# Kernel tuning notes

Measured on AMD Instinct MI355X. Metric: run time of the kernel, lower is better.

Reference implementation:

```python
import jax, jax.numpy as jnp
import numpy as np

SIZE = 416
STRIDES = (8, 16, 32)
A = 3            # anchors per scale
C = 20           # num classes
CONF_THRESH = 0.001
NMS_THRESH = 0.5
ANCHORS = [[1.0,1.5],[2.0,3.0],[3.0,2.5],[1.5,3.5],[3.0,4.0],[4.0,3.0],[3.5,5.0],[5.0,4.5],[8.0,8.0]]


def _make_grids():
    # Mirrors myYOLOv3.init_grid, including the off-by-one that leaves the
    # LAST cell of each scale with zero anchor_wh (slice start:index).
    anchors = np.asarray(ANCHORS, np.float32).reshape(3, 3, 2)
    anchors = anchors * np.array([4.0, 2.0, 1.0], np.float32).reshape(3, 1, 1)
    grids, awhs, strs = [], [], []
    for i, s in enumerate(STRIDES):
        ws, hs = SIZE // s, SIZE // s
        ys, xs = np.meshgrid(np.arange(hs), np.arange(ws), indexing='ij')
        g = np.stack([xs, ys], -1).reshape(hs * ws, 1, 2).astype(np.float32)
        grids.append(np.broadcast_to(g, (hs * ws, A, 2)))
        awh = np.broadcast_to(anchors[i], (hs * ws, A, 2)).copy()
        awh[hs * ws - 1] = 0.0  # replicate init_grid bug
        awhs.append(awh)
        strs.append(np.full((hs * ws, A), s, np.float32))
    grid = jnp.asarray(np.concatenate(grids, 0))      # [HWt, A, 2]
    awh = jnp.asarray(np.concatenate(awhs, 0))        # [HWt, A, 2]
    stride = jnp.asarray(np.concatenate(strs, 0).reshape(-1))  # [HWt*A]
    return grid, awh, stride


def _flatten(pred):
    # [B, A*(1+C+4), H, W] -> obj [B, HW*A], cls [B, HW*A, C], xywh [B, HW, A, 4]
    B, abC, H, W = pred.shape
    p = jnp.transpose(pred, (0, 2, 3, 1)).reshape(B, H * W, abC)
    obj = p[..., :A].reshape(B, H * W * A)
    cls = p[..., A:A * (1 + C)].reshape(B, H * W * A, C)
    xywh = p[..., A * (1 + C):].reshape(B, H * W, A, 4)
    return obj, cls, xywh


def _nms(boxes, scores, cls_inds, valid):
    # Greedy per-class NMS: processing in global score order and suppressing
    # only same-class overlaps is exactly equivalent to the per-class loops
    # in myYOLOv3.postprocess.
    N = boxes.shape[0]
    order = jnp.argsort(-scores)
    b = boxes[order]
    c = cls_inds[order]
    v = valid[order]
    areas = (b[:, 2] - b[:, 0]) * (b[:, 3] - b[:, 1])
    idx = jnp.arange(N)

    def body(i, carry):
        keep, supp = carry
        ki = v[i] & ~supp[i]
        xx1 = jnp.maximum(b[i, 0], b[:, 0])
        yy1 = jnp.maximum(b[i, 1], b[:, 1])
        xx2 = jnp.minimum(b[i, 2], b[:, 2])
        yy2 = jnp.minimum(b[i, 3], b[:, 3])
        inter = jnp.maximum(1e-28, xx2 - xx1) * jnp.maximum(1e-28, yy2 - yy1)
        iou = inter / (areas[i] + areas - inter)
        supp = supp | (ki & (iou > NMS_THRESH) & (c == c[i]) & (idx > i))
        return keep.at[i].set(ki), supp

    keep_s, _ = jax.lax.fori_loop(
        0, N, body, (jnp.zeros(N, bool), jnp.zeros(N, bool)))
    return jnp.zeros(N, bool).at[order].set(keep_s)


def setup_inputs() -> dict:
    key = jax.random.key(0)
    k1, k2, k3 = jax.random.split(key, 3)
    B, abC = 64, A * (1 + 4 + C)
    return {
        'pred_1': jax.random.normal(k1, (B, abC, 52, 52), jnp.float32),
        'pred_2': jax.random.normal(k2, (B, abC, 26, 26), jnp.float32),
        'pred_3': jax.random.normal(k3, (B, abC, 13, 13), jnp.float32),
    }


def reference(pred_1, pred_2, pred_3):
    grid, awh, stride = _make_grids()
    objs, clss, xys = zip(*[_flatten(p) for p in (pred_1, pred_2, pred_3)])
    obj = jnp.concatenate(objs, 1)    # [B, N]
    cls = jnp.concatenate(clss, 1)    # [B, N, C]
    xywh = jnp.concatenate(xys, 1)    # [B, HWt, A, 4]
    B = obj.shape[0]

    # decode_boxes: sigmoid/exp + grid add + stride scale -> xyxy pixels
    cxy = jax.nn.sigmoid(xywh[..., :2]) + grid
    bwh = jnp.exp(xywh[..., 2:]) * awh
    bbox = jnp.concatenate([cxy, bwh], -1).reshape(B, -1, 4)  # [B, N, 4]
    half = bbox[..., 2:] * 0.5
    st = stride[None, :, None]
    boxes = jnp.concatenate([(bbox[..., :2] - half) * st,
                             (bbox[..., :2] + half) * st], -1)  # [B,N,4]

    all_obj = jax.nn.sigmoid(obj[0])                 # [N]
    all_bbox = boxes[0] / SIZE                       # normalized
    all_class = jax.nn.softmax(cls[0], axis=1) * all_obj[:, None]
    cls_inds = jnp.argmax(all_class, axis=1)
    scores = jnp.max(all_class, axis=1)
    valid = scores >= CONF_THRESH

    keep = _nms(all_bbox, scores, cls_inds, valid)

    # bboxes *= scale; clip to [0, SIZE-1]; /= scale
    bboxes = jnp.clip(all_bbox * SIZE, 0.0, SIZE - 1.0) / SIZE
    return bboxes, scores, cls_inds, keep
```

## Files before the change

### kernel.cpp

```cpp
#include <hip/hip_runtime.h>
#include <stdint.h>

typedef unsigned long long u64;
typedef unsigned int u32;

#define NA 10647
#define NCLS 20
#define CAPB 1024
#define CAP2 640
#define NWP 11
#define OUT_SCORES 42588
#define OUT_CLS    53235
#define OUT_KEEP   63882

__constant__ float c_aw[9] = {4.f,8.f,12.f, 3.f,6.f,8.f, 3.5f,5.f,8.f};
__constant__ float c_ah[9] = {6.f,12.f,10.f, 7.f,8.f,6.f, 5.f,4.5f,8.f};

__device__ __forceinline__ float sig(float x){ return 1.0f/(1.0f+expf(-x)); }

__device__ __forceinline__ u64 shflxor64(u64 v, int m){
    int lo = __shfl_xor((int)(u32)(v & 0xffffffffull), m);
    int hi = __shfl_xor((int)(u32)(v >> 32), m);
    return ((u64)(u32)hi << 32) | (u32)lo;
}

__global__ void decode_kernel(const float* __restrict__ p1, const float* __restrict__ p2,
                              const float* __restrict__ p3, float* __restrict__ out,
                              float4* __restrict__ box4, u64* __restrict__ bucket,
                              int* __restrict__ cls_cnt, float* __restrict__ keep_out)
{
    int n = blockIdx.x*256 + threadIdx.x;
    if (n >= NA) return;
    const float* p; int base, W, HW, L; float s;
    if (n < 8112)      { p=p1; base=0;     W=52; HW=2704; s=8.f;  L=0; }
    else if (n<10140)  { p=p2; base=8112;  W=26; HW=676;  s=16.f; L=1; }
    else               { p=p3; base=10140; W=13; HW=169;  s=32.f; L=2; }
    int r  = n - base;
    int hw = r/3, a = r - hw*3;
    int h  = hw/W, w = hw - h*W;

    float obj = sig(p[(size_t)a*HW + hw]);

    float e[NCLS];
    #pragma unroll
    for (int c=0;c<NCLS;c++) e[c] = p[(size_t)(3 + a*NCLS + c)*HW + hw];
    float xmax = e[0];
    #pragma unroll
    for (int c=1;c<NCLS;c++) xmax = fmaxf(xmax, e[c]);
    float ssum = 0.f;
    #pragma unroll
    for (int c=0;c<NCLS;c++){ e[c] = expf(e[c]-xmax); ssum += e[c]; }
    float best = -1.0f; int bi = 0;
    #pragma unroll
    for (int c=0;c<NCLS;c++){ float v = (e[c]/ssum)*obj; if (v > best){ best=v; bi=c; } }

    int xb = 63 + a*4;
    float tx = p[(size_t)(xb+0)*HW + hw];
    float ty = p[(size_t)(xb+1)*HW + hw];
    float tw = p[(size_t)(xb+2)*HW + hw];
    float th = p[(size_t)(xb+3)*HW + hw];
    float aw = c_aw[L*3+a], ah = c_ah[L*3+a];
    if (hw == HW-1){ aw=0.f; ah=0.f; }
    float cx = sig(tx) + (float)w;
    float cy = sig(ty) + (float)h;
    float bw = expf(tw)*aw, bh = expf(th)*ah;
    float hx = bw*0.5f,  hy = bh*0.5f;
    float x1 = ((cx-hx)*s)/416.0f;
    float y1 = ((cy-hy)*s)/416.0f;
    float x2 = ((cx+hx)*s)/416.0f;
    float y2 = ((cy+hy)*s)/416.0f;

    out[n*4+0] = fminf(fmaxf(x1*416.0f,0.f),415.f)/416.0f;
    out[n*4+1] = fminf(fmaxf(y1*416.0f,0.f),415.f)/416.0f;
    out[n*4+2] = fminf(fmaxf(x2*416.0f,0.f),415.f)/416.0f;
    out[n*4+3] = fminf(fmaxf(y2*416.0f,0.f),415.f)/416.0f;
    out[OUT_SCORES + n] = best;
    out[OUT_CLS    + n] = (float)bi;

    box4[n] = make_float4(x1,y1,x2,y2);

    u64 key = ((u64)(~__float_as_uint(best)) << 32) | (u32)n;
    int pos = atomicAdd(&cls_cnt[bi], 1);
    if (pos < CAPB) bucket[(size_t)bi*CAPB + pos] = key;
    else keep_out[n] = 0.0f;
}

__global__ __launch_bounds__(512) void sort_kernel(
    const u64* __restrict__ bucket, const int* __restrict__ cls_cnt,
    const float4* __restrict__ box4, u64* __restrict__ skeys_g,
    float4* __restrict__ sbox_g)
{
    __shared__ u64 lk[CAPB];
    int b = blockIdx.x, tid = threadIdx.x;
    int cnt = cls_cnt[b];
    int Mall = (cnt < CAPB) ? cnt : CAPB;
    int M    = (cnt < CAP2) ? cnt : CAP2;
    for (int t = tid; t < CAPB; t += 512)
        lk[t] = (t < Mall) ? bucket[(size_t)b*CAPB + t] : ~0ull;
    __syncthreads();
    for (int k = 2; k <= CAPB; k <<= 1){
        for (int j = k >> 1; j > 0; j >>= 1){
            int low = tid & (j-1); int i1 = ((tid ^ low) << 1) | low; int i2 = i1 | j;
            bool asc = (i1 & k) == 0;
            u64 A = lk[i1], B = lk[i2];
            if ((A > B) == asc){ lk[i1] = B; lk[i2] = A; }
            __syncthreads();
        }
    }
    for (int t = tid; t < CAPB; t += 512) skeys_g[(size_t)b*CAPB + t] = lk[t];
    for (int t = tid; t < CAP2; t += 512){
        float4 bx = make_float4(0.f,0.f,0.f,0.f);
        if (t < M) bx = box4[(u32)lk[t]];
        sbox_g[(size_t)b*CAP2 + t] = bx;
    }
}

__global__ __launch_bounds__(256) void build_kernel(
    const float4* __restrict__ sbox_g, const int* __restrict__ cls_cnt,
    u64* __restrict__ maskg)
{
    __shared__ float4 cb_s[CAP2];
    __shared__ float  ca_s[CAP2];
    int rc = blockIdx.x, b = blockIdx.y;
    int tid = threadIdx.x, wv = tid>>6, ln = tid&63;
    int cnt = cls_cnt[b];
    int M  = (cnt < CAP2) ? cnt : CAP2;
    int MC = (M + 63) & ~63;
    if (rc*64 >= MC) return;
    for (int t = tid; t < CAP2; t += 256){
        float4 bx = sbox_g[(size_t)b*CAP2 + t];
        cb_s[t] = bx;
        ca_s[t] = (bx.z - bx.x) * (bx.w - bx.y);
    }
    __syncthreads();
    int nw = MC >> 6;
    for (int ri = wv; ri < 64; ri += 4){
        int rrow = rc*64 + ri;
        float4 rb = cb_s[rrow]; float ra = ca_s[rrow];
        for (int w = 0; w < nw; w++){
            int j = w*64 + ln;
            float4 cb = cb_s[j]; float ca = ca_s[j];
            float xx1=fmaxf(rb.x,cb.x), yy1=fmaxf(rb.y,cb.y);
            float xx2=fminf(rb.z,cb.z), yy2=fminf(rb.w,cb.w);
            float inter=fmaxf(1e-28f,xx2-xx1)*fmaxf(1e-28f,yy2-yy1);
            float iou = inter/((ra+ca)-inter);
            u64 bm = __ballot(iou > 0.5f);
            if (ln == 0) maskg[((size_t)b*CAP2 + rrow)*NWP + w] = bm;
        }
    }
}

__global__ __launch_bounds__(512) void scan_kernel(
    const u64* __restrict__ maskg, const u64* __restrict__ skeys_g,
    const int* __restrict__ cls_cnt, float* __restrict__ keep_out)
{
    __shared__ u64 lm[CAP2*NWP];
    __shared__ u64 validw_s[CAP2/64], remw[CAP2/64], keepw_s[CAP2/64];
    __shared__ u64 keep_bc;
    int b = blockIdx.x, tid = threadIdx.x, wv = tid>>6, ln = tid&63;
    int cnt = cls_cnt[b];
    int Mall = (cnt < CAPB) ? cnt : CAPB;
    int M    = (cnt < CAP2) ? cnt : CAP2;
    int MC = (M + 63) & ~63;
    int nw = MC >> 6;

    for (int t = tid; t < MC*NWP; t += 512) lm[t] = maskg[(size_t)b*CAP2*NWP + t];
    for (int w0 = wv; w0 < nw; w0 += 8){
        int t = w0*64 + ln;
        u64 key = skeys_g[(size_t)b*CAPB + t];
        float sc = __uint_as_float(~(u32)(key >> 32));
        u64 bm = __ballot(t < M && sc >= 0.001f);
        if (ln == 0) validw_s[w0] = bm;
    }
    for (int w = tid; w < nw; w += 512) remw[w] = 0ull;
    __syncthreads();

    for (int c = 0; c < nw; c++){
        if (wv == 0){
            u64 W = lm[(c*64 + ln)*NWP + c];
            u64 rem  = remw[c];
            u64 cand = validw_s[c] & ~rem;
            u64 keepw = 0;
            while (cand){
                int bp  = __builtin_ctzll(cand);
                int bps = __builtin_amdgcn_readfirstlane(bp);
                u64 rowm = ((u64)(u32)__builtin_amdgcn_readlane((int)(u32)(W>>32), bps) << 32)
                         |        (u32)__builtin_amdgcn_readlane((int)(u32)(W),     bps);
                keepw |= 1ull << bps;
                cand  &= ~(rowm | (1ull << bps));
            }
            if (ln == 0){ keepw_s[c] = keepw; keep_bc = keepw; }
        }
        __syncthreads();
        u64 kk = keep_bc;
        if (kk && c + 1 < nw){
            int i0 = tid >> 4;
            int wsl = tid & 15;
            int w = c + 1 + wsl;
            u64 acc = 0;
            if (w < nw){
                if ((kk >> i0) & 1ull)        acc  = lm[(c*64 + i0)*NWP + w];
                int i1 = i0 + 32;
                if ((kk >> i1) & 1ull)        acc |= lm[(c*64 + i1)*NWP + w];
            }
            acc |= shflxor64(acc, 16);
            acc |= shflxor64(acc, 32);
            if (ln < 16 && w < nw && acc) atomicOr(&remw[w], acc);
        }
        __syncthreads();
    }

    for (int t = tid; t < Mall; t += 512){
        u32 o = (u32)skeys_g[(size_t)b*CAPB + t];
        float kv = 0.0f;
        if (t < M) kv = ((keepw_s[t>>6] >> (t&63)) & 1ull) ? 1.0f : 0.0f;
        keep_out[o] = kv;
    }
}

extern "C" void kernel_launch(void* const* d_in, const int* in_sizes, int n_in,
                              void* d_out, int out_size, void* d_ws, size_t ws_size,
                              hipStream_t stream) {
    const float* p1 = (const float*)d_in[0];
    const float* p2 = (const float*)d_in[1];
    const float* p3 = (const float*)d_in[2];
    float* out = (float*)d_out;

    char* ws = (char*)d_ws;
    size_t off = 0;
    auto alloc = [&](size_t bytes)->void*{ void* p = ws + off; off += (bytes + 255) & ~(size_t)255; return p; };
    float4* box4    = (float4*)alloc((size_t)NA*16);
    u64*    bucket  = (u64*)   alloc((size_t)NCLS*CAPB*8);
    int*    cls_cnt = (int*)   alloc((size_t)NCLS*4);
    u64*    skeys_g = (u64*)   alloc((size_t)NCLS*CAPB*8);
    float4* sbox_g  = (float4*)alloc((size_t)NCLS*CAP2*16);
    u64*    maskg   = (u64*)   alloc((size_t)NCLS*CAP2*NWP*8);

    hipMemsetAsync(cls_cnt, 0, NCLS*sizeof(int), stream);
    decode_kernel<<<(NA+255)/256, 256, 0, stream>>>(p1,p2,p3,out,box4,bucket,cls_cnt,
                                                    out + OUT_KEEP);
    sort_kernel <<<NCLS, 512, 0, stream>>>(bucket, cls_cnt, box4, skeys_g, sbox_g);
    build_kernel<<<dim3(CAP2/64, NCLS), 256, 0, stream>>>(sbox_g, cls_cnt, maskg);
    scan_kernel <<<NCLS, 512, 0, stream>>>(maskg, skeys_g, cls_cnt, out + OUT_KEEP);
}
```

Baseline: 184.1 us.

## Sort in registers with wave shuffles for small strides, shrink decode blocks

The per-class bitonic sort now keeps one key per thread in a register across 1024 threads. It exchanges via wave64 shuffles for strides up to 32 and goes through shared memory only for larger strides. This removes most __syncthreads barriers and LDS traffic from the 55 compare-exchange steps. Decode blocks also shrink from 256 to 128 threads to spread the work over more blocks. The cost is larger sort blocks and two barriers per shared-memory stage.

After: 181.7 us. Within noise of the previous version (-1.3%).

```diff
diff --git a/kernel.cpp b/kernel.cpp
--- a/kernel.cpp
+++ b/kernel.cpp
@@ -29,7 +29,7 @@
                               float4* __restrict__ box4, u64* __restrict__ bucket,
                               int* __restrict__ cls_cnt, float* __restrict__ keep_out)
 {
-    int n = blockIdx.x*256 + threadIdx.x;
+    int n = blockIdx.x*128 + threadIdx.x;
     if (n >= NA) return;
     const float* p; int base, W, HW, L; float s;
     if (n < 8112)      { p=p1; base=0;     W=52; HW=2704; s=8.f;  L=0; }
@@ -85,32 +85,42 @@
     else keep_out[n] = 0.0f;
 }
 
-__global__ __launch_bounds__(512) void sort_kernel(
+__global__ __launch_bounds__(1024) void sort_kernel(
     const u64* __restrict__ bucket, const int* __restrict__ cls_cnt,
     const float4* __restrict__ box4, u64* __restrict__ skeys_g,
     float4* __restrict__ sbox_g)
 {
-    __shared__ u64 lk[CAPB];
-    int b = blockIdx.x, tid = threadIdx.x;
+    __shared__ u64 ex[CAPB];
+    int b = blockIdx.x, t = threadIdx.x;
     int cnt = cls_cnt[b];
     int Mall = (cnt < CAPB) ? cnt : CAPB;
-    int M    = (cnt < CAP2) ? cnt : CAP2;
-    for (int t = tid; t < CAPB; t += 512)
-        lk[t] = (t < Mall) ? bucket[(size_t)b*CAPB + t] : ~0ull;
-    __syncthreads();
+    u64 v = (t < Mall) ? bucket[(size_t)b*CAPB + t] : ~0ull;
+
+    #pragma unroll
     for (int k = 2; k <= CAPB; k <<= 1){
-        for (int j = k >> 1; j > 0; j >>= 1){
-            int low = tid & (j-1); int i1 = ((tid ^ low) << 1) | low; int i2 = i1 | j;
-            bool asc = (i1 & k) == 0;
-            u64 A = lk[i1], B = lk[i2];
-            if ((A > B) == asc){ lk[i1] = B; lk[i2] = A; }
+        bool asc = ((t & k) == 0);
+        for (int j = k >> 1; j >= 64; j >>= 1){
+            ex[t] = v;
             __syncthreads();
-        }
-    }
-    for (int t = tid; t < CAPB; t += 512) skeys_g[(size_t)b*CAPB + t] = lk[t];
-    for (int t = tid; t < CAP2; t += 512){
+            u64 w = ex[t ^ j];
+            bool takeMin = (((t & j) == 0) == asc);
+            v = takeMin ? (v < w ? v : w) : (v > w ? v : w);
+            __syncthreads();
+        }
+        int j0 = (k >> 1 > 32) ? 32 : (k >> 1);
+        #pragma unroll
+        for (int j = j0; j >= 1; j >>= 1){
+            u64 w = shflxor64(v, j);
+            bool takeMin = (((t & j) == 0) == asc);
+            v = takeMin ? (v < w ? v : w) : (v > w ? v : w);
+        }
+    }
+
+    skeys_g[(size_t)b*CAPB + t] = v;
+    if (t < CAP2){
+        int M = (cnt < CAP2) ? cnt : CAP2;
         float4 bx = make_float4(0.f,0.f,0.f,0.f);
-        if (t < M) bx = box4[(u32)lk[t]];
+        if (t < M) bx = box4[(u32)v];
         sbox_g[(size_t)b*CAP2 + t] = bx;
     }
 }
@@ -237,9 +247,9 @@
     u64*    maskg   = (u64*)   alloc((size_t)NCLS*CAP2*NWP*8);
 
     hipMemsetAsync(cls_cnt, 0, NCLS*sizeof(int), stream);
-    decode_kernel<<<(NA+255)/256, 256, 0, stream>>>(p1,p2,p3,out,box4,bucket,cls_cnt,
+    decode_kernel<<<(NA+127)/128, 128, 0, stream>>>(p1,p2,p3,out,box4,bucket,cls_cnt,
                                                     out + OUT_KEEP);
-    sort_kernel <<<NCLS, 512, 0, stream>>>(bucket, cls_cnt, box4, skeys_g, sbox_g);
+    sort_kernel <<<NCLS, 1024, 0, stream>>>(bucket, cls_cnt, box4, skeys_g, sbox_g);
     build_kernel<<<dim3(CAP2/64, NCLS), 256, 0, stream>>>(sbox_g, cls_cnt, maskg);
     scan_kernel <<<NCLS, 512, 0, stream>>>(maskg, skeys_g, cls_cnt, out + OUT_KEEP);
 }
```
